# Optimization experiments

Hardware: AMD Instinct MI355X
Metric: run time of the kernel (lower is better)

## Reference

```python
import jax, jax.numpy as jnp
import numpy as np

N, M, E, C, F, K = 10000, 20000, 160000, 128, 128, 3
R_CORRECTION = 1.0  # UpsampleModule passes 1 to DPOConv


def setup_inputs() -> dict:
    key = jax.random.key(0)
    ks = jax.random.split(key, 8)
    x = jax.random.normal(ks[0], (N, C), dtype=jnp.float32)
    pos = jax.random.uniform(ks[1], (N, 2), dtype=jnp.float32)
    pos_skip = jax.random.uniform(ks[2], (M, 2), dtype=jnp.float32)
    edge_index = jax.random.randint(ks[3], (2, E), 0, N, dtype=jnp.int64)
    W_conv = jax.random.normal(ks[4], (4 * C, F), dtype=jnp.float32) * 0.02
    b_conv = jnp.zeros((F,), dtype=jnp.float32)
    W2 = jax.random.normal(ks[5], (F, F), dtype=jnp.float32) * 0.02
    b2 = jnp.zeros((F,), dtype=jnp.float32)
    return {"x": x, "pos": pos, "pos_skip": pos_skip, "edge_index": edge_index,
            "W_conv": W_conv, "b_conv": b_conv, "W2": W2, "b2": b2}


def _dpo_conv(x, pos, edge_index, W_conv, b_conv):
    src, dst = edge_index[0], edge_index[1]  # PyG flow: j=source, i=target
    v_j, v_i = x[src], x[dst]                # [E, C]
    diff = pos[dst] - pos[src]               # pos_i - pos_j, [E, 2]
    r2 = jnp.sum(diff * diff, axis=-1)       # [E]
    scale = R_CORRECTION / (r2 + 0.01)       # [E]
    dx = diff[:, 0] * scale
    dy = diff[:, 1] * scale
    v_diff = v_i - v_j
    f = jnp.concatenate([v_diff * dx[:, None], v_diff * dy[:, None], v_j], axis=1)  # [E, 3C]
    agg = jax.ops.segment_sum(f, dst, num_segments=N)
    cnt = jax.ops.segment_sum(jnp.ones((E,), x.dtype), dst, num_segments=N)
    agg = agg / jnp.maximum(cnt, 1.0)[:, None]  # aggr='mean'
    h = jnp.concatenate([agg, x], axis=1) @ W_conv + b_conv  # [N, F]
    return h


def _knn_interpolate(h, pos, pos_skip, k):
    # squared distances target->source, [M, N]
    d2 = jnp.sum((pos_skip[:, None, :] - pos[None, :, :]) ** 2, axis=-1)
    neg_d, idx = jax.lax.top_k(-d2, k)         # k nearest, [M, k]
    w = 1.0 / jnp.maximum(-neg_d, 1e-16)       # inverse squared-distance weights
    return jnp.sum(w[:, :, None] * h[idx], axis=1) / jnp.sum(w, axis=1)[:, None]


def reference(x, pos, pos_skip, edge_index, W_conv, b_conv, W2, b2):
    h = _dpo_conv(x, pos, edge_index, W_conv, b_conv)
    h = jax.nn.elu(h)
    h = jax.nn.elu(h @ W2 + b2)
    return _knn_interpolate(h, pos, pos_skip, K)  # [M, F]
```

## Files before the change

kernel.cpp:

```cpp
#include <hip/hip_runtime.h>
#include <hip/hip_bf16.h>
#include <math.h>
#include <float.h>
#include <stdint.h>

#define N_NODES 10000
#define M_PTS   20000
#define E_EDGES 160000
#define C_CH    128
#define F_CH    128
#define G_GRID  64
#define N_CELLS (G_GRID*G_GRID)
#define NPB     16
#define ECAP    64
#define CCAP    24
#define A_STRIDE 520
#define H_STRIDE 136
#define N_TILES (N_NODES / NPB)
#define W1SZ (4*C_CH*F_CH)
#define W2SZ (F_CH*F_CH)

typedef __attribute__((ext_vector_type(8))) short short8;
typedef __attribute__((ext_vector_type(4))) float f32x4;

__device__ inline ushort f2bf(float v) {
    __hip_bfloat16 b = __float2bfloat16(v);
    return *reinterpret_cast<ushort*>(&b);
}
__device__ inline float bf2f(ushort u) {
    __hip_bfloat16 b = *reinterpret_cast<__hip_bfloat16*>(&u);
    return __bfloat162float(b);
}
__device__ inline float eluf(float v) { return (v > 0.f) ? v : expm1f(v); }
__device__ inline void insert3(uint64_t key, uint64_t& k0, uint64_t& k1, uint64_t& k2) {
    bool lt2 = key < k2, lt1 = key < k1, lt0 = key < k0;
    k2 = lt1 ? k1 : (lt2 ? key : k2);
    k1 = lt0 ? k0 : (lt1 ? key : k1);
    k0 = lt0 ? key : k0;
}

__global__ __launch_bounds__(256) void build_kernel(const int* __restrict__ ei,
    const float* __restrict__ pos, int* __restrict__ ecur, int* __restrict__ ccur,
    int4* __restrict__ edata, int4* __restrict__ cdata,
    const float* __restrict__ Wc, const float* __restrict__ W2,
    ushort* __restrict__ Wct_h, ushort* __restrict__ Wct_l,
    ushort* __restrict__ W2t_h, ushort* __restrict__ W2t_l)
{
    int i = blockIdx.x * 256 + threadIdx.x;
    if (i < E_EDGES) {
        int src = ei[i];
        int dst = ei[E_EDGES + i];
        float dxv = pos[2*dst]     - pos[2*src];
        float dyv = pos[2*dst + 1] - pos[2*src + 1];
        float r2 = dxv*dxv + dyv*dyv;
        float scale = 1.0f / (r2 + 0.01f);
        int slot = atomicAdd(&ecur[dst], 1);
        if (slot < ECAP)
            edata[dst*ECAP + slot] = make_int4(src, __float_as_int(dxv*scale),
                                               __float_as_int(dyv*scale), 0);
    } else if (i < E_EDGES + N_NODES) {
        int j = i - E_EDGES;
        float px = pos[2*j], py = pos[2*j+1];
        int cx = min(max((int)(px * G_GRID), 0), G_GRID - 1);
        int cy = min(max((int)(py * G_GRID), 0), G_GRID - 1);
        int c = cy * G_GRID + cx;
        int slot = atomicAdd(&ccur[c], 1);
        if (slot < CCAP)
            cdata[c*CCAP + slot] = make_int4(__float_as_int(px), __float_as_int(py), j, 0);
    } else if (i < E_EDGES + N_NODES + W1SZ) {
        int j = i - (E_EDGES + N_NODES);
        int n = j >> 9, k = j & 511;
        float v = Wc[k*F_CH + n];
        ushort h = f2bf(v);
        Wct_h[j] = h;
        Wct_l[j] = f2bf(v - bf2f(h));
    } else if (i < E_EDGES + N_NODES + W1SZ + W2SZ) {
        int j = i - (E_EDGES + N_NODES + W1SZ);
        int n = j >> 7, k = j & 127;
        float v = W2[k*F_CH + n];
        ushort h = f2bf(v);
        W2t_h[j] = h;
        W2t_l[j] = f2bf(v - bf2f(h));
    }
}

__global__ __launch_bounds__(1024, 8) void agg_gemm_kernel(const float* __restrict__ x,
    const int* __restrict__ ecur, const int4* __restrict__ edata,
    const ushort* __restrict__ Wct_h, const ushort* __restrict__ Wct_l,
    const ushort* __restrict__ W2t_h, const ushort* __restrict__ W2t_l,
    const float* __restrict__ bc, const float* __restrict__ b2,
    float* __restrict__ h2out)
{
    __shared__ alignas(16) ushort sA_h[NPB * A_STRIDE];
    __shared__ alignas(16) ushort sA_l[NPB * A_STRIDE];
    __shared__ alignas(16) ushort sH_h[NPB * H_STRIDE];
    __shared__ alignas(16) ushort sH_l[NPB * H_STRIDE];

    const int tid = threadIdx.x;
    const int lane = tid & 63;
    const int wave = tid >> 6;
    const int nodeBase = blockIdx.x * NPB;
    const float2* xv = (const float2*)x;

    {
        const int rr = wave;
        int node = nodeBase + rr;
        float2 xi = xv[(size_t)node*64 + lane];
        int cnt = ecur[node];
        int m = min(cnt, ECAP);
        int4 er = edata[(size_t)node*ECAP + lane];
        double a1x = 0., a1y = 0., a2x = 0., a2y = 0., a3x = 0., a3y = 0.;
        int p = 0;
        for (; p + 3 < m; p += 4) {
            int s0 = __shfl(er.x, p);     int s1 = __shfl(er.x, p+1);
            int s2 = __shfl(er.x, p+2);   int s3 = __shfl(er.x, p+3);
            float dx0 = __int_as_float(__shfl(er.y, p));
            float dy0 = __int_as_float(__shfl(er.z, p));
            float dx1 = __int_as_float(__shfl(er.y, p+1));
            float dy1 = __int_as_float(__shfl(er.z, p+1));
            float dx2 = __int_as_float(__shfl(er.y, p+2));
            float dy2 = __int_as_float(__shfl(er.z, p+2));
            float dx3 = __int_as_float(__shfl(er.y, p+3));
            float dy3 = __int_as_float(__shfl(er.z, p+3));
            float2 x0 = xv[(size_t)s0*64 + lane];
            float2 x1 = xv[(size_t)s1*64 + lane];
            float2 x2 = xv[(size_t)s2*64 + lane];
            float2 x3 = xv[(size_t)s3*64 + lane];
            float vx0 = xi.x - x0.x, vy0 = xi.y - x0.y;
            float vx1 = xi.x - x1.x, vy1 = xi.y - x1.y;
            float vx2 = xi.x - x2.x, vy2 = xi.y - x2.y;
            float vx3 = xi.x - x3.x, vy3 = xi.y - x3.y;
            a1x += (double)(vx0*dx0); a1y += (double)(vy0*dx0);
            a2x += (double)(vx0*dy0); a2y += (double)(vy0*dy0);
            a3x += (double)x0.x;      a3y += (double)x0.y;
            a1x += (double)(vx1*dx1); a1y += (double)(vy1*dx1);
            a2x += (double)(vx1*dy1); a2y += (double)(vy1*dy1);
            a3x += (double)x1.x;      a3y += (double)x1.y;
            a1x += (double)(vx2*dx2); a1y += (double)(vy2*dx2);
            a2x += (double)(vx2*dy2); a2y += (double)(vy2*dy2);
            a3x += (double)x2.x;      a3y += (double)x2.y;
            a1x += (double)(vx3*dx3); a1y += (double)(vy3*dx3);
            a2x += (double)(vx3*dy3); a2y += (double)(vy3*dy3);
            a3x += (double)x3.x;      a3y += (double)x3.y;
        }
        for (; p < m; p++) {
            int s = __shfl(er.x, p);
            float dxe = __int_as_float(__shfl(er.y, p));
            float dye = __int_as_float(__shfl(er.z, p));
            float2 xj = xv[(size_t)s*64 + lane];
            float vx = xi.x - xj.x, vy = xi.y - xj.y;
            a1x += (double)(vx*dxe); a1y += (double)(vy*dxe);
            a2x += (double)(vx*dye); a2y += (double)(vy*dye);
            a3x += (double)xj.x;     a3y += (double)xj.y;
        }
        float inv = 1.0f / fmaxf((float)cnt, 1.0f);
        float vals[4][2] = {{(float)a1x*inv, (float)a1y*inv},
                            {(float)a2x*inv, (float)a2y*inv},
                            {(float)a3x*inv, (float)a3y*inv},
                            {xi.x, xi.y}};
        int b = rr * A_STRIDE;
        int c0 = 2*lane;
        #pragma unroll
        for (int seg = 0; seg < 4; seg++) {
            ushort hx = f2bf(vals[seg][0]), hy = f2bf(vals[seg][1]);
            ushort lx = f2bf(vals[seg][0] - bf2f(hx)), ly = f2bf(vals[seg][1] - bf2f(hy));
            *(uint*)&sA_h[b + seg*128 + c0] = (uint)hx | ((uint)hy << 16);
            *(uint*)&sA_l[b + seg*128 + c0] = (uint)lx | ((uint)ly << 16);
        }
    }
    __syncthreads();

    const int col16 = lane & 15;
    const int quad  = lane >> 4;
    const int row   = col16;
    const int ncol  = (wave & 7)*16 + col16;

    if (wave < 8) {
        const float bcv = bc[ncol];
        f32x4 acc = {0,0,0,0};
        for (int ks = 0; ks < 16; ks++) {
            int kb = ks*32 + quad*8;
            short8 ah = *(const short8*)&sA_h[row*A_STRIDE + kb];
            short8 al = *(const short8*)&sA_l[row*A_STRIDE + kb];
            short8 bh = *(const short8*)(Wct_h + (size_t)ncol*512 + kb);
            short8 bl = *(const short8*)(Wct_l + (size_t)ncol*512 + kb);
            acc = __builtin_amdgcn_mfma_f32_16x16x32_bf16(ah, bh, acc, 0, 0, 0);
            acc = __builtin_amdgcn_mfma_f32_16x16x32_bf16(ah, bl, acc, 0, 0, 0);
            acc = __builtin_amdgcn_mfma_f32_16x16x32_bf16(al, bh, acc, 0, 0, 0);
        }
        #pragma unroll
        for (int r = 0; r < 4; r++) {
            int rr = quad*4 + r;
            float v = eluf(acc[r] + bcv);
            ushort hh = f2bf(v);
            sH_h[rr*H_STRIDE + ncol] = hh;
            sH_l[rr*H_STRIDE + ncol] = f2bf(v - bf2f(hh));
        }
    }
    __syncthreads();

    if (wave < 8) {
        const float b2v = b2[ncol];
        f32x4 acc2 = {0,0,0,0};
        for (int ks = 0; ks < 4; ks++) {
            int kb = ks*32 + quad*8;
            short8 ah = *(const short8*)&sH_h[row*H_STRIDE + kb];
            short8 al = *(const short8*)&sH_l[row*H_STRIDE + kb];
            short8 bh = *(const short8*)(W2t_h + ncol*128 + kb);
            short8 bl = *(const short8*)(W2t_l + ncol*128 + kb);
            acc2 = __builtin_amdgcn_mfma_f32_16x16x32_bf16(ah, bh, acc2, 0, 0, 0);
            acc2 = __builtin_amdgcn_mfma_f32_16x16x32_bf16(ah, bl, acc2, 0, 0, 0);
            acc2 = __builtin_amdgcn_mfma_f32_16x16x32_bf16(al, bh, acc2, 0, 0, 0);
        }
        #pragma unroll
        for (int r = 0; r < 4; r++) {
            int node = nodeBase + quad*4 + r;
            float v = eluf(acc2[r] + b2v);
            h2out[(size_t)node*F_CH + ncol] = v;
        }
    }
}

__global__ __launch_bounds__(256) void knn_gather_kernel(const float* __restrict__ pos_skip,
    const int* __restrict__ ccur, const int4* __restrict__ cdata,
    const float* __restrict__ h2, float* __restrict__ out)
{
    int gt = blockIdx.x * 256 + threadIdx.x;
    if (gt >= M_PTS*8) return;
    int t = gt >> 3;
    int sub = gt & 7;
    float tx = pos_skip[2*t], ty = pos_skip[2*t+1];
    const float h = 1.0f / G_GRID;
    int cx = min(max((int)(tx * G_GRID), 0), G_GRID - 1);
    int cy = min(max((int)(ty * G_GRID), 0), G_GRID - 1);

    uint64_t k0 = UINT64_MAX, k1 = UINT64_MAX, k2 = UINT64_MAX;
    uint64_t m0 = UINT64_MAX, m1 = UINT64_MAX, m2 = UINT64_MAX;

    for (int r = 0; ; r++) {
        if (r > 0) {
            m0 = k0; m1 = k1; m2 = k2;
            #pragma unroll
            for (int m = 1; m <= 4; m <<= 1) {
                uint64_t p0 = __shfl_xor((unsigned long long)m0, m, 64);
                uint64_t p1 = __shfl_xor((unsigned long long)m1, m, 64);
                uint64_t p2 = __shfl_xor((unsigned long long)m2, m, 64);
                insert3(p0, m0, m1, m2);
                insert3(p1, m0, m1, m2);
                insert3(p2, m0, m1, m2);
            }
            float bound = ((r - 1) * h) * ((r - 1) * h) * 0.99999f;
            float d2cur = __uint_as_float((uint32_t)(m2 >> 32));
            if (d2cur < bound || r >= G_GRID) break;
        }
        int x0 = max(cx - r, 0), x1 = min(cx + r, G_GRID - 1);
        int y0 = max(cy - r, 0), y1 = min(cy + r, G_GRID - 1);
        int cidx = 0;
        for (int yy = y0; yy <= y1; yy++) {
            bool yedge = (yy == cy - r) || (yy == cy + r);
            for (int xx = x0; xx <= x1; xx++) {
                if (r > 0 && !yedge && xx != cx - r && xx != cx + r) continue;
                if ((cidx++ & 7) != sub) continue;
                int c = yy * G_GRID + xx;
                int pc = min(ccur[c], CCAP);
                const int4* cb = cdata + c*CCAP;
                for (int p = 0; p < pc; p++) {
                    int4 sp = cb[p];
                    float ddx = __fadd_rn(__int_as_float(sp.x), -tx);
                    float ddy = __fadd_rn(__int_as_float(sp.y), -ty);
                    float dd = __fadd_rn(__fmul_rn(ddx, ddx), __fmul_rn(ddy, ddy));
                    uint64_t key = ((uint64_t)__float_as_uint(dd) << 32) | (uint32_t)sp.z;
                    insert3(key, k0, k1, k2);
                }
            }
        }
    }

    float d0 = __uint_as_float((uint32_t)(m0 >> 32));
    float d1 = __uint_as_float((uint32_t)(m1 >> 32));
    float d2 = __uint_as_float((uint32_t)(m2 >> 32));
    float w0 = 1.0f / fmaxf(d0, 1e-16f);
    float w1 = 1.0f / fmaxf(d1, 1e-16f);
    float w2 = 1.0f / fmaxf(d2, 1e-16f);
    float wsum = w0 + w1 + w2;
    w0 /= wsum; w1 /= wsum; w2 /= wsum;
    int j0 = (int)(uint32_t)m0, j1 = (int)(uint32_t)m1, j2 = (int)(uint32_t)m2;
    const float4* r0 = (const float4*)(h2 + (size_t)j0*F_CH);
    const float4* r1 = (const float4*)(h2 + (size_t)j1*F_CH);
    const float4* r2 = (const float4*)(h2 + (size_t)j2*F_CH);
    float4* ot = (float4*)(out + (size_t)t*F_CH);
    #pragma unroll
    for (int q = 0; q < 4; q++) {
        int idx = sub*4 + q;
        float4 a = r0[idx], b = r1[idx], c = r2[idx];
        float4 v;
        v.x = w0*a.x + w1*b.x + w2*c.x;
        v.y = w0*a.y + w1*b.y + w2*c.y;
        v.z = w0*a.z + w1*b.z + w2*c.z;
        v.w = w0*a.w + w1*b.w + w2*c.w;
        ot[idx] = v;
    }
}

extern "C" void kernel_launch(void* const* d_in, const int* in_sizes, int n_in,
                              void* d_out, int out_size, void* d_ws, size_t ws_size,
                              hipStream_t stream) {
    const float* x        = (const float*)d_in[0];
    const float* pos      = (const float*)d_in[1];
    const float* pos_skip = (const float*)d_in[2];
    const int*   ei       = (const int*)  d_in[3];
    const float* Wc       = (const float*)d_in[4];
    const float* bc       = (const float*)d_in[5];
    const float* W2       = (const float*)d_in[6];
    const float* b2       = (const float*)d_in[7];
    float* out = (float*)d_out;

    char* ws = (char*)d_ws;
    size_t off = 0;
    auto alloc = [&](size_t bytes) {
        void* p = ws + off;
        off = (off + bytes + 255) & ~(size_t)255;
        return p;
    };
    int*    ecur   = (int*)   alloc((size_t)N_NODES * 4);
    int*    ccur   = (int*)   alloc((size_t)N_CELLS * 4);
    size_t  cur_bytes = (size_t)((char*)ccur - (char*)ecur) + (size_t)N_CELLS * 4;
    int4*   edata  = (int4*)  alloc((size_t)N_NODES * ECAP * 16);
    int4*   cdata  = (int4*)  alloc((size_t)N_CELLS * CCAP * 16);
    float*  h2     = (float*) alloc((size_t)N_NODES * F_CH * 4);
    ushort* Wct_h  = (ushort*)alloc((size_t)F_CH * 512 * 2);
    ushort* Wct_l  = (ushort*)alloc((size_t)F_CH * 512 * 2);
    ushort* W2t_h  = (ushort*)alloc((size_t)F_CH * 128 * 2);
    ushort* W2t_l  = (ushort*)alloc((size_t)F_CH * 128 * 2);

    hipMemsetAsync(ecur, 0, cur_bytes, stream);
    const int TOT = E_EDGES + N_NODES + W1SZ + W2SZ;
    build_kernel<<<(TOT + 255) / 256, 256, 0, stream>>>(ei, pos, ecur, ccur, edata, cdata,
                                                        Wc, W2, Wct_h, Wct_l, W2t_h, W2t_l);
    agg_gemm_kernel<<<N_TILES, 1024, 0, stream>>>(x, ecur, edata,
        Wct_h, Wct_l, W2t_h, W2t_l, bc, b2, h2);
    knn_gather_kernel<<<(M_PTS*8 + 255) / 256, 256, 0, stream>>>(pos_skip, ccur, cdata, h2, out);
}
```

Measured before the change: 161.0 us.

## Co-schedule KNN search with aggregation GEMM blocks; split out weighted gather

The KNN grid search moves into the aggregation/GEMM kernel as every fifth block, so the neighbour search runs alongside the edge aggregation and MLP instead of after it. The search writes indices and normalized weights to a workspace, and a small separate kernel then does the weighted gather of h2 rows with one wave per output point. The search also skips the termination check at ring 1 and always scans rings 0 and 1. This trades an extra launch and a small index/weight buffer for overlap between the two independent phases, but mixing divergent search blocks with 1024-thread MFMA blocks may upset load balance.

```diff
diff --git a/kernel.cpp b/kernel.cpp
--- a/kernel.cpp
+++ b/kernel.cpp
@@ -17,6 +17,7 @@
 #define A_STRIDE 520
 #define H_STRIDE 136
 #define N_TILES (N_NODES / NPB)
+#define N_KNNB  157
 #define W1SZ (4*C_CH*F_CH)
 #define W2SZ (F_CH*F_CH)
 
@@ -84,22 +85,99 @@
     }
 }
 
-__global__ __launch_bounds__(1024, 8) void agg_gemm_kernel(const float* __restrict__ x,
+__global__ __launch_bounds__(1024, 8) void mega_kernel(const float* __restrict__ x,
     const int* __restrict__ ecur, const int4* __restrict__ edata,
     const ushort* __restrict__ Wct_h, const ushort* __restrict__ Wct_l,
     const ushort* __restrict__ W2t_h, const ushort* __restrict__ W2t_l,
     const float* __restrict__ bc, const float* __restrict__ b2,
-    float* __restrict__ h2out)
+    float* __restrict__ h2out,
+    const float* __restrict__ pos_skip, const int* __restrict__ ccur,
+    const int4* __restrict__ cdata,
+    int* __restrict__ knn_idx, float* __restrict__ knn_w)
 {
     __shared__ alignas(16) ushort sA_h[NPB * A_STRIDE];
     __shared__ alignas(16) ushort sA_l[NPB * A_STRIDE];
     __shared__ alignas(16) ushort sH_h[NPB * H_STRIDE];
     __shared__ alignas(16) ushort sH_l[NPB * H_STRIDE];
 
+    const int bid = blockIdx.x;
     const int tid = threadIdx.x;
     const int lane = tid & 63;
     const int wave = tid >> 6;
-    const int nodeBase = blockIdx.x * NPB;
+
+    if (bid % 5 == 4) {
+        int gt = (bid / 5) * 1024 + tid;
+        if (gt >= M_PTS * 8) return;
+        int t = gt >> 3;
+        int sub = gt & 7;
+        float tx = pos_skip[2*t], ty = pos_skip[2*t+1];
+        const float h = 1.0f / G_GRID;
+        int cx = min(max((int)(tx * G_GRID), 0), G_GRID - 1);
+        int cy = min(max((int)(ty * G_GRID), 0), G_GRID - 1);
+
+        uint64_t k0 = UINT64_MAX, k1 = UINT64_MAX, k2 = UINT64_MAX;
+        uint64_t m0 = UINT64_MAX, m1 = UINT64_MAX, m2 = UINT64_MAX;
+
+        for (int r = 0; ; r++) {
+            if (r >= 2) {
+                m0 = k0; m1 = k1; m2 = k2;
+                #pragma unroll
+                for (int m = 1; m <= 4; m <<= 1) {
+                    uint64_t p0 = __shfl_xor((unsigned long long)m0, m, 64);
+                    uint64_t p1 = __shfl_xor((unsigned long long)m1, m, 64);
+                    uint64_t p2 = __shfl_xor((unsigned long long)m2, m, 64);
+                    insert3(p0, m0, m1, m2);
+                    insert3(p1, m0, m1, m2);
+                    insert3(p2, m0, m1, m2);
+                }
+                float bound = ((r - 1) * h) * ((r - 1) * h) * 0.99999f;
+                float d2cur = __uint_as_float((uint32_t)(m2 >> 32));
+                if (d2cur < bound || r >= G_GRID) break;
+            }
+            int x0 = max(cx - r, 0), x1 = min(cx + r, G_GRID - 1);
+            int y0 = max(cy - r, 0), y1 = min(cy + r, G_GRID - 1);
+            int cidx = 0;
+            for (int yy = y0; yy <= y1; yy++) {
+                bool yedge = (yy == cy - r) || (yy == cy + r);
+                for (int xx = x0; xx <= x1; xx++) {
+                    if (r > 0 && !yedge && xx != cx - r && xx != cx + r) continue;
+                    if ((cidx++ & 7) != sub) continue;
+                    int c = yy * G_GRID + xx;
+                    int pc = min(ccur[c], CCAP);
+                    const int4* cb = cdata + c*CCAP;
+                    for (int p = 0; p < pc; p++) {
+                        int4 sp = cb[p];
+                        float ddx = __fadd_rn(__int_as_float(sp.x), -tx);
+                        float ddy = __fadd_rn(__int_as_float(sp.y), -ty);
+                        float dd = __fadd_rn(__fmul_rn(ddx, ddx), __fmul_rn(ddy, ddy));
+                        uint64_t key = ((uint64_t)__float_as_uint(dd) << 32) | (uint32_t)sp.z;
+                        insert3(key, k0, k1, k2);
+                    }
+                }
+            }
+        }
+
+        if (sub == 0) {
+            float d0 = __uint_as_float((uint32_t)(m0 >> 32));
+            float d1 = __uint_as_float((uint32_t)(m1 >> 32));
+            float d2 = __uint_as_float((uint32_t)(m2 >> 32));
+            float w0 = 1.0f / fmaxf(d0, 1e-16f);
+            float w1 = 1.0f / fmaxf(d1, 1e-16f);
+            float w2 = 1.0f / fmaxf(d2, 1e-16f);
+            float wsum = w0 + w1 + w2;
+            knn_idx[t*3+0] = (int)(uint32_t)m0;
+            knn_idx[t*3+1] = (int)(uint32_t)m1;
+            knn_idx[t*3+2] = (int)(uint32_t)m2;
+            knn_w[t*3+0] = w0 / wsum;
+            knn_w[t*3+1] = w1 / wsum;
+            knn_w[t*3+2] = w2 / wsum;
+        }
+        return;
+    }
+
+    const int agg_id = bid - bid / 5;
+    if (agg_id >= N_TILES) return;
+    const int nodeBase = agg_id * NPB;
     const float2* xv = (const float2*)x;
 
     {
@@ -221,85 +299,20 @@
     }
 }
 
-__global__ __launch_bounds__(256) void knn_gather_kernel(const float* __restrict__ pos_skip,
-    const int* __restrict__ ccur, const int4* __restrict__ cdata,
-    const float* __restrict__ h2, float* __restrict__ out)
+__global__ __launch_bounds__(256) void gather_kernel(const float* __restrict__ h2,
+    const int* __restrict__ knn_idx, const float* __restrict__ knn_w,
+    float* __restrict__ out)
 {
-    int gt = blockIdx.x * 256 + threadIdx.x;
-    if (gt >= M_PTS*8) return;
-    int t = gt >> 3;
-    int sub = gt & 7;
-    float tx = pos_skip[2*t], ty = pos_skip[2*t+1];
-    const float h = 1.0f / G_GRID;
-    int cx = min(max((int)(tx * G_GRID), 0), G_GRID - 1);
-    int cy = min(max((int)(ty * G_GRID), 0), G_GRID - 1);
-
-    uint64_t k0 = UINT64_MAX, k1 = UINT64_MAX, k2 = UINT64_MAX;
-    uint64_t m0 = UINT64_MAX, m1 = UINT64_MAX, m2 = UINT64_MAX;
-
-    for (int r = 0; ; r++) {
-        if (r > 0) {
-            m0 = k0; m1 = k1; m2 = k2;
-            #pragma unroll
-            for (int m = 1; m <= 4; m <<= 1) {
-                uint64_t p0 = __shfl_xor((unsigned long long)m0, m, 64);
-                uint64_t p1 = __shfl_xor((unsigned long long)m1, m, 64);
-                uint64_t p2 = __shfl_xor((unsigned long long)m2, m, 64);
-                insert3(p0, m0, m1, m2);
-                insert3(p1, m0, m1, m2);
-                insert3(p2, m0, m1, m2);
-            }
-            float bound = ((r - 1) * h) * ((r - 1) * h) * 0.99999f;
-            float d2cur = __uint_as_float((uint32_t)(m2 >> 32));
-            if (d2cur < bound || r >= G_GRID) break;
-        }
-        int x0 = max(cx - r, 0), x1 = min(cx + r, G_GRID - 1);
-        int y0 = max(cy - r, 0), y1 = min(cy + r, G_GRID - 1);
-        int cidx = 0;
-        for (int yy = y0; yy <= y1; yy++) {
-            bool yedge = (yy == cy - r) || (yy == cy + r);
-            for (int xx = x0; xx <= x1; xx++) {
-                if (r > 0 && !yedge && xx != cx - r && xx != cx + r) continue;
-                if ((cidx++ & 7) != sub) continue;
-                int c = yy * G_GRID + xx;
-                int pc = min(ccur[c], CCAP);
-                const int4* cb = cdata + c*CCAP;
-                for (int p = 0; p < pc; p++) {
-                    int4 sp = cb[p];
-                    float ddx = __fadd_rn(__int_as_float(sp.x), -tx);
-                    float ddy = __fadd_rn(__int_as_float(sp.y), -ty);
-                    float dd = __fadd_rn(__fmul_rn(ddx, ddx), __fmul_rn(ddy, ddy));
-                    uint64_t key = ((uint64_t)__float_as_uint(dd) << 32) | (uint32_t)sp.z;
-                    insert3(key, k0, k1, k2);
-                }
-            }
-        }
-    }
-
-    float d0 = __uint_as_float((uint32_t)(m0 >> 32));
-    float d1 = __uint_as_float((uint32_t)(m1 >> 32));
-    float d2 = __uint_as_float((uint32_t)(m2 >> 32));
-    float w0 = 1.0f / fmaxf(d0, 1e-16f);
-    float w1 = 1.0f / fmaxf(d1, 1e-16f);
-    float w2 = 1.0f / fmaxf(d2, 1e-16f);
-    float wsum = w0 + w1 + w2;
-    w0 /= wsum; w1 /= wsum; w2 /= wsum;
-    int j0 = (int)(uint32_t)m0, j1 = (int)(uint32_t)m1, j2 = (int)(uint32_t)m2;
-    const float4* r0 = (const float4*)(h2 + (size_t)j0*F_CH);
-    const float4* r1 = (const float4*)(h2 + (size_t)j1*F_CH);
-    const float4* r2 = (const float4*)(h2 + (size_t)j2*F_CH);
-    float4* ot = (float4*)(out + (size_t)t*F_CH);
-    #pragma unroll
-    for (int q = 0; q < 4; q++) {
-        int idx = sub*4 + q;
-        float4 a = r0[idx], b = r1[idx], c = r2[idx];
-        float4 v;
-        v.x = w0*a.x + w1*b.x + w2*c.x;
-        v.y = w0*a.y + w1*b.y + w2*c.y;
-        v.z = w0*a.z + w1*b.z + w2*c.z;
-        v.w = w0*a.w + w1*b.w + w2*c.w;
-        ot[idx] = v;
-    }
+    int m = blockIdx.x * 4 + (threadIdx.x >> 6);
+    int lane = threadIdx.x & 63;
+    const float2* h2v = (const float2*)h2;
+    int j0 = knn_idx[m*3+0], j1 = knn_idx[m*3+1], j2 = knn_idx[m*3+2];
+    float w0 = knn_w[m*3+0], w1 = knn_w[m*3+1], w2 = knn_w[m*3+2];
+    float2 a = h2v[(size_t)j0*64 + lane], b = h2v[(size_t)j1*64 + lane], c = h2v[(size_t)j2*64 + lane];
+    float2 v;
+    v.x = w0*a.x + w1*b.x + w2*c.x;
+    v.y = w0*a.y + w1*b.y + w2*c.y;
+    ((float2*)out)[(size_t)m*64 + lane] = v;
 }
 
 extern "C" void kernel_launch(void* const* d_in, const int* in_sizes, int n_in,
@@ -322,22 +335,25 @@
         off = (off + bytes + 255) & ~(size_t)255;
         return p;
     };
-    int*    ecur   = (int*)   alloc((size_t)N_NODES * 4);
-    int*    ccur   = (int*)   alloc((size_t)N_CELLS * 4);
+    int*    ecur    = (int*)   alloc((size_t)N_NODES * 4);
+    int*    ccur    = (int*)   alloc((size_t)N_CELLS * 4);
     size_t  cur_bytes = (size_t)((char*)ccur - (char*)ecur) + (size_t)N_CELLS * 4;
-    int4*   edata  = (int4*)  alloc((size_t)N_NODES * ECAP * 16);
-    int4*   cdata  = (int4*)  alloc((size_t)N_CELLS * CCAP * 16);
-    float*  h2     = (float*) alloc((size_t)N_NODES * F_CH * 4);
-    ushort* Wct_h  = (ushort*)alloc((size_t)F_CH * 512 * 2);
-    ushort* Wct_l  = (ushort*)alloc((size_t)F_CH * 512 * 2);
-    ushort* W2t_h  = (ushort*)alloc((size_t)F_CH * 128 * 2);
-    ushort* W2t_l  = (ushort*)alloc((size_t)F_CH * 128 * 2);
+    int4*   edata   = (int4*)  alloc((size_t)N_NODES * ECAP * 16);
+    int4*   cdata   = (int4*)  alloc((size_t)N_CELLS * CCAP * 16);
+    float*  h2      = (float*) alloc((size_t)N_NODES * F_CH * 4);
+    int*    knn_idx = (int*)   alloc((size_t)M_PTS * 3 * 4);
+    float*  knn_w   = (float*) alloc((size_t)M_PTS * 3 * 4);
+    ushort* Wct_h   = (ushort*)alloc((size_t)F_CH * 512 * 2);
+    ushort* Wct_l   = (ushort*)alloc((size_t)F_CH * 512 * 2);
+    ushort* W2t_h   = (ushort*)alloc((size_t)F_CH * 128 * 2);
+    ushort* W2t_l   = (ushort*)alloc((size_t)F_CH * 128 * 2);
 
     hipMemsetAsync(ecur, 0, cur_bytes, stream);
     const int TOT = E_EDGES + N_NODES + W1SZ + W2SZ;
     build_kernel<<<(TOT + 255) / 256, 256, 0, stream>>>(ei, pos, ecur, ccur, edata, cdata,
                                                         Wc, W2, Wct_h, Wct_l, W2t_h, W2t_l);
-    agg_gemm_kernel<<<N_TILES, 1024, 0, stream>>>(x, ecur, edata,
-        Wct_h, Wct_l, W2t_h, W2t_l, bc, b2, h2);
-    knn_gather_kernel<<<(M_PTS*8 + 255) / 256, 256, 0, stream>>>(pos_skip, ccur, cdata, h2, out);
-}
+    mega_kernel<<<785, 1024, 0, stream>>>(x, ecur, edata,
+        Wct_h, Wct_l, W2t_h, W2t_l, bc, b2, h2,
+        pos_skip, ccur, cdata, knn_idx, knn_w);
+    gather_kernel<<<M_PTS / 4, 256, 0, stream>>>(h2, knn_idx, knn_w, out);
+}
```

Measured after the change: 157.0 us. 2.5% less time.
